# Performance work log

Hardware: AMD Instinct MI355X
Metric: run time of the kernel (lower is better)

Reference implementation:

```python
import jax, jax.numpy as jnp
import numpy as np

B, C, H, W = 8, 128, 256, 256
L = 3          # wt_levels
K = 5          # depthwise conv kernel size
DN = ('NCHW', 'OIHW', 'NCHW')


def _haar_filters(c):
    # pywt 'db1': dec_lo=[s,s], dec_hi=[-s,s]; code reverses dec filters;
    # rec filters are reversed then flipped back -> original.
    s = np.float32(1.0 / np.sqrt(2.0))
    dec_lo = np.array([s, s], np.float32)    # dec_lo[::-1]
    dec_hi = np.array([s, -s], np.float32)   # dec_hi[::-1]
    rec_lo = np.array([s, s], np.float32)
    rec_hi = np.array([s, -s], np.float32)
    # torch: a.unsqueeze(0)*b.unsqueeze(1) == outer(b, a)
    dec = np.stack([np.outer(dec_lo, dec_lo), np.outer(dec_hi, dec_lo),
                    np.outer(dec_lo, dec_hi), np.outer(dec_hi, dec_hi)])  # (4,2,2)
    rec = np.stack([np.outer(rec_lo, rec_lo), np.outer(rec_hi, rec_lo),
                    np.outer(rec_lo, rec_hi), np.outer(rec_hi, rec_hi)])
    dec = np.tile(dec[:, None], (c, 1, 1, 1))  # (4c,1,2,2), torch .repeat tiling
    rec = np.tile(rec[:, None], (c, 1, 1, 1))
    return jnp.asarray(dec), jnp.asarray(rec)


def _dw(x, w, pad):
    # depthwise conv, stride 1; w: (Cout,1,k,k), groups = x channels
    return jax.lax.conv_general_dilated(x, w, (1, 1), pad,
                                        feature_group_count=x.shape[1],
                                        dimension_numbers=DN)


def _wt(x, filt):
    # F.conv2d(x, filt, stride=2, groups=c, padding=0) for 2x2 db1 filters
    b, c, h, w = x.shape
    y = jax.lax.conv_general_dilated(x, filt, (2, 2), ((0, 0), (0, 0)),
                                     feature_group_count=c,
                                     dimension_numbers=DN)
    return y.reshape(b, c, 4, h // 2, w // 2)


def _iwt(x5, rec):
    # F.conv_transpose2d(x, rec, stride=2, groups=c, padding=0), rec: (4c,1,2,2)
    b, c, _, h, w = x5.shape
    x = x5.reshape(b, 4 * c, h, w)
    k = rec.reshape(c, 4, 2, 2)[:, :, ::-1, ::-1]  # OIHW, spatially flipped
    return jax.lax.conv_general_dilated(x, k, (1, 1), ((1, 1), (1, 1)),
                                        lhs_dilation=(2, 2),
                                        feature_group_count=c,
                                        dimension_numbers=DN)


def setup_inputs() -> dict:
    key = jax.random.key(0)
    ks = jax.random.split(key, 6)
    wt_filter, iwt_filter = _haar_filters(C)
    return {
        'x': jax.random.normal(ks[0], (B, C, H, W), jnp.float32),
        'wt_filter': wt_filter,
        'iwt_filter': iwt_filter,
        'base_w': jax.random.normal(ks[1], (C, 1, K, K), jnp.float32) * 0.05,
        'base_b': jax.random.normal(ks[2], (C,), jnp.float32) * 0.05,
        'base_scale': jnp.ones((1, C, 1, 1), jnp.float32)
                      + jax.random.normal(ks[3], (1, C, 1, 1), jnp.float32) * 0.02,
        'wconv_w': jax.random.normal(ks[4], (L, 4 * C, 1, K, K), jnp.float32) * 0.05,
        'wscale': 0.1 * jnp.ones((L, 1, 4 * C, 1, 1), jnp.float32)
                  + jax.random.normal(ks[5], (L, 1, 4 * C, 1, 1), jnp.float32) * 0.01,
    }


def reference(x, wt_filter, iwt_filter, base_w, base_b, base_scale, wconv_w, wscale):
    p = base_w.shape[-1] // 2
    SAME = ((p, p), (p, p))
    levels = wconv_w.shape[0]
    ll_in, h_in, shapes = [], [], []
    curr = x
    for i in range(levels):
        shapes.append(curr.shape)
        ph, pw = curr.shape[2] % 2, curr.shape[3] % 2
        if ph or pw:
            curr = jnp.pad(curr, ((0, 0), (0, 0), (0, ph), (0, pw)))
        c5 = _wt(curr, wt_filter)                       # (b,c,4,h/2,w/2)
        curr = c5[:, :, 0]                              # LL band
        b, c, _, hh, ww = c5.shape
        tag = c5.reshape(b, 4 * c, hh, ww)
        tag = wscale[i] * _dw(tag, wconv_w[i], SAME)    # depthwise conv + scale
        tag = tag.reshape(b, c, 4, hh, ww)
        ll_in.append(tag[:, :, 0])
        h_in.append(tag[:, :, 1:4])
    next_ll = jnp.zeros((), x.dtype)
    for i in range(levels - 1, -1, -1):
        cur = jnp.concatenate([(ll_in[i] + next_ll)[:, :, None], h_in[i]], axis=2)
        next_ll = _iwt(cur, iwt_filter)
        sh = shapes[i]
        next_ll = next_ll[:, :, :sh[2], :sh[3]]
    base = base_scale * (_dw(x, base_w, SAME) + base_b[None, :, None, None])
    return base + next_ll
```

## Files before the change

kernel.cpp:

```cpp
#include <hip/hip_runtime.h>

#define BB 8
#define CC 128
#define HH 256
#define WW 256

template <int H, int W>
__global__ __launch_bounds__(256) void fwd_level_kernel(
    const float* __restrict__ in,
    const float* __restrict__ wconv,
    const float* __restrict__ wsc,
    float* __restrict__ tag,
    float* __restrict__ rawLL)
{
    constexpr int hh = H / 2, ww = W / 2;
    const int bc  = blockIdx.z;
    const int c   = bc % CC;
    const int ti0 = blockIdx.y * 16;
    const int tj0 = blockIdx.x * 16;
    const int tid = threadIdx.x;

    __shared__ float sb[4][20][20];
    __shared__ float wg[4][25];
    __shared__ float wsl[4];

    if (tid < 100) {
        int k = tid / 25, t = tid % 25;
        wg[k][t] = wconv[(c * 4 + k) * 25 + t];
    }
    if (tid < 4) wsl[tid] = wsc[c * 4 + tid];

    const float* inb = in + (size_t)bc * H * W;

    for (int idx = tid; idx < 400; idx += 256) {
        int r = idx / 20, q = idx % 20;
        int si = ti0 - 2 + r, sj = tj0 - 2 + q;
        float c0 = 0.f, c1 = 0.f, c2 = 0.f, c3 = 0.f;
        if (si >= 0 && si < hh && sj >= 0 && sj < ww) {
            const float* p = inb + (size_t)(2 * si) * W + 2 * sj;
            float x00 = p[0], x01 = p[1], x10 = p[W], x11 = p[W + 1];
            c0 = 0.5f * (x00 + x01 + x10 + x11);
            c1 = 0.5f * (x00 + x01 - x10 - x11);
            c2 = 0.5f * (x00 - x01 + x10 - x11);
            c3 = 0.5f * (x00 - x01 - x10 + x11);
        }
        sb[0][r][q] = c0; sb[1][r][q] = c1; sb[2][r][q] = c2; sb[3][r][q] = c3;
    }
    __syncthreads();

    const int ty = tid / 16, tx = tid % 16;
    const int i = ti0 + ty, j = tj0 + tx;

    float outv[4];
#pragma unroll
    for (int k = 0; k < 4; ++k) {
        float acc = 0.f;
#pragma unroll
        for (int u = 0; u < 5; ++u)
#pragma unroll
            for (int v = 0; v < 5; ++v)
                acc += sb[k][ty + u][tx + v] * wg[k][u * 5 + v];
        outv[k] = wsl[k] * acc;
    }

    const size_t plane = (size_t)hh * ww;
    const size_t tbase = (size_t)bc * 4 * plane + (size_t)i * ww + j;
#pragma unroll
    for (int k = 0; k < 4; ++k)
        tag[tbase + (size_t)k * plane] = outv[k];

    if (rawLL)
        rawLL[(size_t)bc * plane + (size_t)i * ww + j] = sb[0][ty + 2][tx + 2];
}

__global__ __launch_bounds__(256) void ll0_kernel(
    const float* __restrict__ x, float* __restrict__ ll)
{
    int gid = blockIdx.x * 256 + threadIdx.x;
    int t  = gid & 4095;
    int bc = gid >> 12;
    int i  = t >> 5;
    int j4 = (t & 31) << 2;
    const float* p = x + (size_t)bc * 65536 + (size_t)(2 * i) * 256 + 2 * j4;
    float4 a0 = *(const float4*)p;
    float4 a1 = *(const float4*)(p + 4);
    float4 b0 = *(const float4*)(p + 256);
    float4 b1 = *(const float4*)(p + 260);
    float4 r;
    r.x = 0.5f * (a0.x + a0.y + b0.x + b0.y);
    r.y = 0.5f * (a0.z + a0.w + b0.z + b0.w);
    r.z = 0.5f * (a1.x + a1.y + b1.x + b1.y);
    r.w = 0.5f * (a1.z + a1.w + b1.z + b1.w);
    *(float4*)(ll + (size_t)bc * 16384 + i * 128 + j4) = r;
}

__global__ __launch_bounds__(256) void final2_kernel(
    const float* __restrict__ x,
    const float* __restrict__ tag1,
    const float* __restrict__ tag2,
    const float* __restrict__ wconv0,
    const float* __restrict__ wsc0,
    const float* __restrict__ base_w,
    const float* __restrict__ base_b,
    const float* __restrict__ base_scale,
    float* __restrict__ out)
{
    const int bc  = blockIdx.z;
    const int c   = bc % CC;
    const int tY0 = blockIdx.y * 32, tX0 = blockIdx.x * 32;
    const int tid = threadIdx.x;

    __shared__ float sx[40][42];
    __shared__ float scf[4][20][22];
    __shared__ float scv[4][16][17];
    __shared__ float sll1[16][17];
    __shared__ float st1[4][8][9];
    __shared__ float sll2[8][9];
    __shared__ float wb[25];
    __shared__ float w0[4][25];
    __shared__ float wsl[4];
    __shared__ float sbias, sscale;

    if (tid < 25) wb[tid] = base_w[c * 25 + tid];
    if (tid >= 32 && tid < 132) {
        int t = tid - 32;
        w0[t / 25][t % 25] = wconv0[(c * 4 + t / 25) * 25 + t % 25];
    }
    if (tid >= 160 && tid < 164) wsl[tid - 160] = wsc0[c * 4 + (tid - 160)];
    if (tid == 255) { sbias = base_b[c]; sscale = base_scale[c]; }

    const float* xb = x + (size_t)bc * (HH * WW);
    for (int idx = tid; idx < 1600; idx += 256) {
        int r = idx / 40, q = idx - r * 40;
        int Y = tY0 - 4 + r, X = tX0 - 4 + q;
        sx[r][q] = (Y >= 0 && Y < HH && X >= 0 && X < WW)
                       ? xb[Y * WW + X] : 0.f;
    }

    const int t1r0 = tY0 >> 2, t1c0 = tX0 >> 2;
    const float* t1b = tag1 + (size_t)bc * 4 * 4096;
    {
        int k = tid >> 6, t = tid & 63, r = t >> 3, q = t & 7;
        st1[k][r][q] = t1b[k * 4096 + (t1r0 + r) * 64 + (t1c0 + q)];
    }

    const int t2r0 = tY0 >> 3, t2c0 = tX0 >> 3;
    const float* t2b = tag2 + (size_t)bc * 4 * 1024;
    if (tid < 64) {
        int r = tid >> 3, q = tid & 7;
        const float* p = t2b + (t2r0 + (r >> 1)) * 32 + (t2c0 + (q >> 1));
        float d0 = p[0], d1 = p[1024], d2 = p[2048], d3 = p[3072];
        float ss = (r & 1) ? -1.f : 1.f, tt = (q & 1) ? -1.f : 1.f;
        sll2[r][q] = 0.5f * (d0 + ss * d1 + tt * d2 + ss * tt * d3);
    }
    __syncthreads();

    for (int idx = tid; idx < 400; idx += 256) {
        int r = idx / 20, q = idx - r * 20;
        float x00 = sx[2 * r][2 * q],     x01 = sx[2 * r][2 * q + 1];
        float x10 = sx[2 * r + 1][2 * q], x11 = sx[2 * r + 1][2 * q + 1];
        scf[0][r][q] = 0.5f * (x00 + x01 + x10 + x11);
        scf[1][r][q] = 0.5f * (x00 + x01 - x10 - x11);
        scf[2][r][q] = 0.5f * (x00 - x01 + x10 - x11);
        scf[3][r][q] = 0.5f * (x00 - x01 - x10 + x11);
    }
    {
        int ci = tid >> 4, cj = tid & 15;
        int a = ci >> 1, b = cj >> 1;
        float e0 = st1[0][a][b] + sll2[a][b];
        float e1 = st1[1][a][b], e2 = st1[2][a][b], e3 = st1[3][a][b];
        float ss = (ci & 1) ? -1.f : 1.f, tt = (cj & 1) ? -1.f : 1.f;
        sll1[ci][cj] = 0.5f * (e0 + ss * e1 + tt * e2 + ss * tt * e3);
    }
    __syncthreads();

    {
        int k = tid >> 6, t = tid & 63, g = t >> 4, cx = t & 15;
        float accb[4] = {0.f, 0.f, 0.f, 0.f};
#pragma unroll
        for (int v = 0; v < 5; ++v)
#pragma unroll
            for (int i = 0; i < 8; ++i) {
                float val = scf[k][4 * g + i][cx + v];
#pragma unroll
                for (int r = 0; r < 4; ++r) {
                    int u = i - r;
                    if (u >= 0 && u < 5) accb[r] += val * w0[k][u * 5 + v];
                }
            }
        float wk = wsl[k];
#pragma unroll
        for (int r = 0; r < 4; ++r) scv[k][4 * g + r][cx] = wk * accb[r];
    }

    const int ty = tid >> 5, tx = tid & 31;
    float accx[4] = {0.f, 0.f, 0.f, 0.f};
#pragma unroll
    for (int v = 0; v < 5; ++v)
#pragma unroll
        for (int i = 0; i < 8; ++i) {
            float val = sx[4 * ty + i + 2][tx + v + 2];
#pragma unroll
            for (int r = 0; r < 4; ++r) {
                int u = i - r;
                if (u >= 0 && u < 5) accx[r] += val * wb[u * 5 + v];
            }
        }
    __syncthreads();

    float* ob = out + (size_t)bc * (HH * WW);
    const int Ybase = tY0 + 4 * ty;
    const int cx = tx >> 1;
    const float sbn = (tx & 1) ? -1.f : 1.f;
#pragma unroll
    for (int half = 0; half < 2; ++half) {
        int cy = 2 * ty + half;
        float c0 = scv[0][cy][cx] + sll1[cy][cx];
        float c1 = scv[1][cy][cx];
        float c2 = scv[2][cy][cx];
        float c3 = scv[3][cy][cx];
        float e = c0 + sbn * c2;
        float o = c1 + sbn * c3;
        float w_even = 0.5f * (e + o);
        float w_odd  = 0.5f * (e - o);
        int r0 = 2 * half;
        ob[(Ybase + r0) * WW + tX0 + tx] =
            sscale * (accx[r0] + sbias) + w_even;
        ob[(Ybase + r0 + 1) * WW + tX0 + tx] =
            sscale * (accx[r0 + 1] + sbias) + w_odd;
    }
}

extern "C" void kernel_launch(void* const* d_in, const int* in_sizes, int n_in,
                              void* d_out, int out_size, void* d_ws, size_t ws_size,
                              hipStream_t stream)
{
    const float* x          = (const float*)d_in[0];
    const float* base_w     = (const float*)d_in[3];
    const float* base_b     = (const float*)d_in[4];
    const float* base_scale = (const float*)d_in[5];
    const float* wconv      = (const float*)d_in[6];
    const float* wscale     = (const float*)d_in[7];
    float* out = (float*)d_out;
    float* ws  = (float*)d_ws;

    float* rawLL0 = ws;
    float* tag1   = ws + 16777216;
    float* rawLL1 = ws + 33554432;
    float* tag2   = ws + 37748736;

    const dim3 blk(256);
    const int BC = BB * CC;

    ll0_kernel<<<dim3(16384), blk, 0, stream>>>(x, rawLL0);

    fwd_level_kernel<128, 128><<<dim3(4, 4, BC), blk, 0, stream>>>(
        rawLL0, wconv + 512 * 25, wscale + 512, tag1, rawLL1);
    fwd_level_kernel<64, 64><<<dim3(2, 2, BC), blk, 0, stream>>>(
        rawLL1, wconv + 2 * 512 * 25, wscale + 2 * 512, tag2, nullptr);

    final2_kernel<<<dim3(8, 8, BC), blk, 0, stream>>>(
        x, tag1, tag2, wconv, wscale, base_w, base_b, base_scale, out);
}
```

Baseline: 813.2 us.

## Fuse level-0 LL computation into level-1 forward kernel and vectorize loads

```diff
diff --git a/kernel.cpp b/kernel.cpp
--- a/kernel.cpp
+++ b/kernel.cpp
@@ -5,96 +5,163 @@
 #define HH 256
 #define WW 256
 
-template <int H, int W>
-__global__ __launch_bounds__(256) void fwd_level_kernel(
-    const float* __restrict__ in,
+__global__ __launch_bounds__(256, 4) void fwd1_fused_kernel(
+    const float* __restrict__ x,
     const float* __restrict__ wconv,
     const float* __restrict__ wsc,
     float* __restrict__ tag,
-    float* __restrict__ rawLL)
+    float* __restrict__ rawLL1)
 {
-    constexpr int hh = H / 2, ww = W / 2;
     const int bc  = blockIdx.z;
     const int c   = bc % CC;
-    const int ti0 = blockIdx.y * 16;
-    const int tj0 = blockIdx.x * 16;
+    const int ti0 = blockIdx.y * 32, tj0 = blockIdx.x * 32;
     const int tid = threadIdx.x;
 
-    __shared__ float sb[4][20][20];
+    __shared__ float sb[4][36][38];
     __shared__ float wg[4][25];
     __shared__ float wsl[4];
 
-    if (tid < 100) {
-        int k = tid / 25, t = tid % 25;
-        wg[k][t] = wconv[(c * 4 + k) * 25 + t];
-    }
+    if (tid < 100) { int k = tid / 25, t = tid % 25;
+                     wg[k][t] = wconv[(c * 4 + k) * 25 + t]; }
     if (tid < 4) wsl[tid] = wsc[c * 4 + tid];
 
-    const float* inb = in + (size_t)bc * H * W;
-
-    for (int idx = tid; idx < 400; idx += 256) {
-        int r = idx / 20, q = idx % 20;
+    const float* xb = x + (size_t)bc * (HH * WW);
+    for (int idx = tid; idx < 36 * 36; idx += 256) {
+        int r = idx / 36, q = idx - r * 36;
         int si = ti0 - 2 + r, sj = tj0 - 2 + q;
         float c0 = 0.f, c1 = 0.f, c2 = 0.f, c3 = 0.f;
-        if (si >= 0 && si < hh && sj >= 0 && sj < ww) {
-            const float* p = inb + (size_t)(2 * si) * W + 2 * sj;
-            float x00 = p[0], x01 = p[1], x10 = p[W], x11 = p[W + 1];
-            c0 = 0.5f * (x00 + x01 + x10 + x11);
-            c1 = 0.5f * (x00 + x01 - x10 - x11);
-            c2 = 0.5f * (x00 - x01 + x10 - x11);
-            c3 = 0.5f * (x00 - x01 - x10 + x11);
+        if (si >= 0 && si < 64 && sj >= 0 && sj < 64) {
+            const float* p = xb + (size_t)(4 * si) * WW + 4 * sj;
+            float4 r0 = *(const float4*)p;
+            float4 r1 = *(const float4*)(p + WW);
+            float4 r2 = *(const float4*)(p + 2 * WW);
+            float4 r3 = *(const float4*)(p + 3 * WW);
+            float q00 = r0.x + r0.y + r1.x + r1.y;
+            float q01 = r0.z + r0.w + r1.z + r1.w;
+            float q10 = r2.x + r2.y + r3.x + r3.y;
+            float q11 = r2.z + r2.w + r3.z + r3.w;
+            float s0 = q00 + q01, d0 = q00 - q01;
+            float s1 = q10 + q11, d1 = q10 - q11;
+            c0 = 0.25f * (s0 + s1);
+            c1 = 0.25f * (s0 - s1);
+            c2 = 0.25f * (d0 + d1);
+            c3 = 0.25f * (d0 - d1);
         }
         sb[0][r][q] = c0; sb[1][r][q] = c1; sb[2][r][q] = c2; sb[3][r][q] = c3;
     }
     __syncthreads();
 
-    const int ty = tid / 16, tx = tid % 16;
-    const int i = ti0 + ty, j = tj0 + tx;
-
-    float outv[4];
-#pragma unroll
-    for (int k = 0; k < 4; ++k) {
-        float acc = 0.f;
-#pragma unroll
-        for (int u = 0; u < 5; ++u)
-#pragma unroll
-            for (int v = 0; v < 5; ++v)
-                acc += sb[k][ty + u][tx + v] * wg[k][u * 5 + v];
-        outv[k] = wsl[k] * acc;
-    }
-
-    const size_t plane = (size_t)hh * ww;
-    const size_t tbase = (size_t)bc * 4 * plane + (size_t)i * ww + j;
-#pragma unroll
-    for (int k = 0; k < 4; ++k)
-        tag[tbase + (size_t)k * plane] = outv[k];
-
-    if (rawLL)
-        rawLL[(size_t)bc * plane + (size_t)i * ww + j] = sb[0][ty + 2][tx + 2];
+    const int k  = tid >> 6, t = tid & 63;
+    const int gh = t >> 5, cx = t & 31;
+    float wr[25];
+#pragma unroll
+    for (int t2 = 0; t2 < 25; ++t2) wr[t2] = wg[k][t2];
+    const float wk = wsl[k];
+    const size_t plane = 64 * 64;
+    float* tb = tag + (size_t)bc * 4 * plane + (size_t)k * plane;
+
+#pragma unroll
+    for (int rr = 0; rr < 4; ++rr) {
+        const int row0 = 16 * gh + 4 * rr;
+        float acc[4] = {0.f, 0.f, 0.f, 0.f};
+#pragma unroll
+        for (int v = 0; v < 5; ++v)
+#pragma unroll
+            for (int i = 0; i < 8; ++i) {
+                float val = sb[k][row0 + i][cx + v];
+#pragma unroll
+                for (int r = 0; r < 4; ++r) {
+                    int u = i - r;
+                    if (u >= 0 && u < 5) acc[r] += val * wr[u * 5 + v];
+                }
+            }
+#pragma unroll
+        for (int r = 0; r < 4; ++r)
+            tb[(size_t)(ti0 + row0 + r) * 64 + (tj0 + cx)] = wk * acc[r];
+    }
+
+    for (int idx = tid; idx < 1024; idx += 256) {
+        int r = idx >> 5, q = idx & 31;
+        rawLL1[(size_t)bc * plane + (size_t)(ti0 + r) * 64 + (tj0 + q)] =
+            sb[0][r + 2][q + 2];
+    }
 }
 
-__global__ __launch_bounds__(256) void ll0_kernel(
-    const float* __restrict__ x, float* __restrict__ ll)
+__global__ __launch_bounds__(256, 4) void fwd2_kernel(
+    const float* __restrict__ ll,
+    const float* __restrict__ wconv,
+    const float* __restrict__ wsc,
+    float* __restrict__ tag)
 {
-    int gid = blockIdx.x * 256 + threadIdx.x;
-    int t  = gid & 4095;
-    int bc = gid >> 12;
-    int i  = t >> 5;
-    int j4 = (t & 31) << 2;
-    const float* p = x + (size_t)bc * 65536 + (size_t)(2 * i) * 256 + 2 * j4;
-    float4 a0 = *(const float4*)p;
-    float4 a1 = *(const float4*)(p + 4);
-    float4 b0 = *(const float4*)(p + 256);
-    float4 b1 = *(const float4*)(p + 260);
-    float4 r;
-    r.x = 0.5f * (a0.x + a0.y + b0.x + b0.y);
-    r.y = 0.5f * (a0.z + a0.w + b0.z + b0.w);
-    r.z = 0.5f * (a1.x + a1.y + b1.x + b1.y);
-    r.w = 0.5f * (a1.z + a1.w + b1.z + b1.w);
-    *(float4*)(ll + (size_t)bc * 16384 + i * 128 + j4) = r;
+    const int bc  = blockIdx.x;
+    const int c   = bc % CC;
+    const int tid = threadIdx.x;
+
+    __shared__ float sb[4][36][38];
+    __shared__ float wg[4][25];
+    __shared__ float wsl[4];
+
+    if (tid < 100) { int k = tid / 25, t = tid % 25;
+                     wg[k][t] = wconv[(c * 4 + k) * 25 + t]; }
+    if (tid < 4) wsl[tid] = wsc[c * 4 + tid];
+
+    const float* lb = ll + (size_t)bc * 4096;
+    for (int idx = tid; idx < 36 * 18; idx += 256) {
+        int r = idx / 18, u = idx - r * 18;
+        int si = -2 + r, sj0 = -2 + 2 * u;
+        float c00 = 0.f, c10 = 0.f, c20 = 0.f, c30 = 0.f;
+        float c01 = 0.f, c11 = 0.f, c21 = 0.f, c31 = 0.f;
+        if (si >= 0 && si < 32 && sj0 >= 0 && sj0 < 32) {
+            const float* p = lb + (size_t)(2 * si) * 64 + 2 * sj0;
+            float4 a = *(const float4*)p;
+            float4 b = *(const float4*)(p + 64);
+            c00 = 0.5f * (a.x + a.y + b.x + b.y);
+            c10 = 0.5f * (a.x + a.y - b.x - b.y);
+            c20 = 0.5f * (a.x - a.y + b.x - b.y);
+            c30 = 0.5f * (a.x - a.y - b.x + b.y);
+            c01 = 0.5f * (a.z + a.w + b.z + b.w);
+            c11 = 0.5f * (a.z + a.w - b.z - b.w);
+            c21 = 0.5f * (a.z - a.w + b.z - b.w);
+            c31 = 0.5f * (a.z - a.w - b.z + b.w);
+        }
+        int q0 = 2 * u;
+        sb[0][r][q0] = c00; sb[1][r][q0] = c10;
+        sb[2][r][q0] = c20; sb[3][r][q0] = c30;
+        sb[0][r][q0 + 1] = c01; sb[1][r][q0 + 1] = c11;
+        sb[2][r][q0 + 1] = c21; sb[3][r][q0 + 1] = c31;
+    }
+    __syncthreads();
+
+    const int k  = tid >> 6, t = tid & 63;
+    const int gh = t >> 5, cx = t & 31;
+    float wr[25];
+#pragma unroll
+    for (int t2 = 0; t2 < 25; ++t2) wr[t2] = wg[k][t2];
+    const float wk = wsl[k];
+    float* tb = tag + (size_t)bc * 4096 + (size_t)k * 1024;
+
+#pragma unroll
+    for (int rr = 0; rr < 4; ++rr) {
+        const int row0 = 16 * gh + 4 * rr;
+        float acc[4] = {0.f, 0.f, 0.f, 0.f};
+#pragma unroll
+        for (int v = 0; v < 5; ++v)
+#pragma unroll
+            for (int i = 0; i < 8; ++i) {
+                float val = sb[k][row0 + i][cx + v];
+#pragma unroll
+                for (int r = 0; r < 4; ++r) {
+                    int u = i - r;
+                    if (u >= 0 && u < 5) acc[r] += val * wr[u * 5 + v];
+                }
+            }
+#pragma unroll
+        for (int r = 0; r < 4; ++r)
+            tb[(size_t)(row0 + r) * 32 + cx] = wk * acc[r];
+    }
 }
 
-__global__ __launch_bounds__(256) void final2_kernel(
+__global__ __launch_bounds__(256, 4) void final2_kernel(
     const float* __restrict__ x,
     const float* __restrict__ tag1,
     const float* __restrict__ tag2,
@@ -110,7 +177,7 @@
     const int tY0 = blockIdx.y * 32, tX0 = blockIdx.x * 32;
     const int tid = threadIdx.x;
 
-    __shared__ float sx[40][42];
+    __shared__ float sx[40][44];
     __shared__ float scf[4][20][22];
     __shared__ float scv[4][16][17];
     __shared__ float sll1[16][17];
@@ -130,11 +197,13 @@
     if (tid == 255) { sbias = base_b[c]; sscale = base_scale[c]; }
 
     const float* xb = x + (size_t)bc * (HH * WW);
-    for (int idx = tid; idx < 1600; idx += 256) {
-        int r = idx / 40, q = idx - r * 40;
-        int Y = tY0 - 4 + r, X = tX0 - 4 + q;
-        sx[r][q] = (Y >= 0 && Y < HH && X >= 0 && X < WW)
-                       ? xb[Y * WW + X] : 0.f;
+    for (int idx = tid; idx < 400; idx += 256) {
+        int r = idx / 10, q4 = idx - r * 10;
+        int Y = tY0 - 4 + r, X0 = tX0 - 4 + 4 * q4;
+        float4 v = make_float4(0.f, 0.f, 0.f, 0.f);
+        if (Y >= 0 && Y < HH && X0 >= 0 && X0 < WW)
+            v = *(const float4*)(xb + (size_t)Y * WW + X0);
+        *(float4*)&sx[r][4 * q4] = v;
     }
 
     const int t1r0 = tY0 >> 2, t1c0 = tX0 >> 2;
@@ -176,6 +245,9 @@
 
     {
         int k = tid >> 6, t = tid & 63, g = t >> 4, cx = t & 15;
+        float wr[25];
+#pragma unroll
+        for (int t2 = 0; t2 < 25; ++t2) wr[t2] = w0[k][t2];
         float accb[4] = {0.f, 0.f, 0.f, 0.f};
 #pragma unroll
         for (int v = 0; v < 5; ++v)
@@ -185,7 +257,7 @@
 #pragma unroll
                 for (int r = 0; r < 4; ++r) {
                     int u = i - r;
-                    if (u >= 0 && u < 5) accb[r] += val * w0[k][u * 5 + v];
+                    if (u >= 0 && u < 5) accb[r] += val * wr[u * 5 + v];
                 }
             }
         float wk = wsl[k];
@@ -194,6 +266,9 @@
     }
 
     const int ty = tid >> 5, tx = tid & 31;
+    float wbr[25];
+#pragma unroll
+    for (int t2 = 0; t2 < 25; ++t2) wbr[t2] = wb[t2];
     float accx[4] = {0.f, 0.f, 0.f, 0.f};
 #pragma unroll
     for (int v = 0; v < 5; ++v)
@@ -203,7 +278,7 @@
 #pragma unroll
             for (int r = 0; r < 4; ++r) {
                 int u = i - r;
-                if (u >= 0 && u < 5) accx[r] += val * wb[u * 5 + v];
+                if (u >= 0 && u < 5) accx[r] += val * wbr[u * 5 + v];
             }
         }
     __syncthreads();
@@ -224,9 +299,9 @@
         float w_even = 0.5f * (e + o);
         float w_odd  = 0.5f * (e - o);
         int r0 = 2 * half;
-        ob[(Ybase + r0) * WW + tX0 + tx] =
+        ob[(size_t)(Ybase + r0) * WW + tX0 + tx] =
             sscale * (accx[r0] + sbias) + w_even;
-        ob[(Ybase + r0 + 1) * WW + tX0 + tx] =
+        ob[(size_t)(Ybase + r0 + 1) * WW + tX0 + tx] =
             sscale * (accx[r0 + 1] + sbias) + w_odd;
     }
 }
@@ -244,20 +319,18 @@
     float* out = (float*)d_out;
     float* ws  = (float*)d_ws;
 
-    float* rawLL0 = ws;
-    float* tag1   = ws + 16777216;
-    float* rawLL1 = ws + 33554432;
-    float* tag2   = ws + 37748736;
+    float* tag1   = ws;
+    float* rawLL1 = ws + 16777216;
+    float* tag2   = ws + 20971520;
 
     const dim3 blk(256);
     const int BC = BB * CC;
 
-    ll0_kernel<<<dim3(16384), blk, 0, stream>>>(x, rawLL0);
-
-    fwd_level_kernel<128, 128><<<dim3(4, 4, BC), blk, 0, stream>>>(
-        rawLL0, wconv + 512 * 25, wscale + 512, tag1, rawLL1);
-    fwd_level_kernel<64, 64><<<dim3(2, 2, BC), blk, 0, stream>>>(
-        rawLL1, wconv + 2 * 512 * 25, wscale + 2 * 512, tag2, nullptr);
+    fwd1_fused_kernel<<<dim3(2, 2, BC), blk, 0, stream>>>(
+        x, wconv + 512 * 25, wscale + 512, tag1, rawLL1);
+
+    fwd2_kernel<<<dim3(BC), blk, 0, stream>>>(
+        rawLL1, wconv + 2 * 512 * 25, wscale + 2 * 512, tag2);
 
     final2_kernel<<<dim3(8, 8, BC), blk, 0, stream>>>(
         x, tag1, tag2, wconv, wscale, base_w, base_b, base_scale, out);
```

Result: faster. 690.5 us (-15.1%).
